# Kernel tuning notes

Hardware: AMD Instinct MI355X
Metric: run time of the kernel (lower is better)

The kernel has to match this reference:

```python
import jax, jax.numpy as jnp
import numpy as np

N_NODES = 50000
N_EDGES = 800000
IN_DIM = 128
HID = 64
HEADS = 4
OUT_DIM = 128
NEG_SLOPE = 0.2


def setup_inputs() -> dict:
    key = jax.random.key(0)
    ks = jax.random.split(key, 11)
    x = jax.random.normal(ks[0], (N_NODES, IN_DIM), dtype=jnp.float32)
    edge_index = jax.random.randint(ks[1], (2, N_EDGES), 0, N_NODES, dtype=jnp.int64)
    s1 = 1.0 / np.sqrt(IN_DIM)
    s2 = 1.0 / np.sqrt(HEADS * HID)
    W1 = jax.random.normal(ks[2], (IN_DIM, HEADS * HID), dtype=jnp.float32) * s1
    a_src1 = jax.random.normal(ks[3], (HEADS, HID), dtype=jnp.float32) * s2
    a_dst1 = jax.random.normal(ks[4], (HEADS, HID), dtype=jnp.float32) * s2
    b1 = jnp.zeros((HEADS * HID,), dtype=jnp.float32)
    W2 = jax.random.normal(ks[5], (HEADS * HID, OUT_DIM), dtype=jnp.float32) * s2
    a_src2 = jax.random.normal(ks[6], (1, OUT_DIM), dtype=jnp.float32) * 0.1
    a_dst2 = jax.random.normal(ks[7], (1, OUT_DIM), dtype=jnp.float32) * 0.1
    b2 = jnp.zeros((OUT_DIM,), dtype=jnp.float32)
    return {"x": x, "edge_index": edge_index, "W1": W1, "a_src1": a_src1,
            "a_dst1": a_dst1, "b1": b1, "W2": W2, "a_src2": a_src2,
            "a_dst2": a_dst2, "b2": b2}


def _gat_conv(x, src, dst, W, a_src, a_dst, bias, heads, out_per_head, concat):
    n = x.shape[0]
    # linear projection per head: [N, H, F]
    h = (x @ W).reshape(n, heads, out_per_head)
    # per-node attention terms: [N, H]
    alpha_src = jnp.einsum('nhf,hf->nh', h, a_src)
    alpha_dst = jnp.einsum('nhf,hf->nh', h, a_dst)
    # edge logits with LeakyReLU: [E, H]
    e = jax.nn.leaky_relu(alpha_src[src] + alpha_dst[dst], NEG_SLOPE)
    # softmax over incoming edges of each destination node
    m = jax.ops.segment_max(e, dst, num_segments=n)  # [N, H]
    m = jnp.where(jnp.isfinite(m), m, 0.0)
    e = jnp.exp(e - m[dst])
    denom = jax.ops.segment_sum(e, dst, num_segments=n)  # [N, H]
    alpha = e / (denom[dst] + 1e-16)  # [E, H]
    # weighted scatter-aggregate of source messages
    out = jax.ops.segment_sum(h[src] * alpha[:, :, None], dst, num_segments=n)  # [N, H, F]
    if concat:
        out = out.reshape(n, heads * out_per_head)
    else:
        out = out.mean(axis=1)
    return out + bias


def reference(x, edge_index, W1, a_src1, a_dst1, b1, W2, a_src2, a_dst2, b2):
    n = x.shape[0]
    # PyG GATConv adds self-loops by default
    loops = jnp.arange(n, dtype=edge_index.dtype)
    src = jnp.concatenate([edge_index[0], loops])
    dst = jnp.concatenate([edge_index[1], loops])
    # dropout layers are identity in inference
    h = _gat_conv(x, src, dst, W1, a_src1, a_dst1, b1, HEADS, HID, True)
    h = jax.nn.elu(h)
    out = _gat_conv(h, src, dst, W2, a_src2, a_dst2, b2, 1, OUT_DIM, True)
    # F.normalize(p=2, dim=1)
    norm = jnp.linalg.norm(out, axis=1, keepdims=True)
    return out / jnp.maximum(norm, 1e-12)
```

## Files before the change

### kernel.cpp

```cpp
#include <hip/hip_runtime.h>
#include <hip/hip_fp16.h>
#include <math.h>

#define N_NODES 50000
#define N_EDGES 800000
#define ET (N_EDGES + N_NODES)
#define IN_DIM 128
#define HID 64
#define HEADS 4
#define C1 (HEADS * HID)
#define OUT_DIM 128
#define NEG_SLOPE 0.2f
#define MTILES 3125
#define SCAN_B 1024
#define NSCB 49

typedef _Float16 h8 __attribute__((ext_vector_type(8)));
typedef float f4 __attribute__((ext_vector_type(4)));
typedef unsigned short u16;

__device__ __forceinline__ float leaky(float v) { return fmaxf(v, NEG_SLOPE * v); }
__device__ __forceinline__ float elu(float v) { return v > 0.0f ? v : expm1f(v); }

__device__ __forceinline__ void fma_mix8(float* acc, h8 v, float w) {
    union { h8 h; int i[4]; } u; u.h = v;
#pragma unroll
    for (int k = 0; k < 4; ++k) {
        asm("v_fma_mix_f32 %0, %1, %2, %0 op_sel:[0,0,0] op_sel_hi:[1,0,0]"
            : "+v"(acc[2 * k]) : "v"(u.i[k]), "v"(w));
        asm("v_fma_mix_f32 %0, %1, %2, %0 op_sel:[1,0,0] op_sel_hi:[1,0,0]"
            : "+v"(acc[2 * k + 1]) : "v"(u.i[k]), "v"(w));
    }
}

__global__ void prep_kernel(const float* __restrict__ W1, const float* __restrict__ W2,
                            const int* __restrict__ dst, __half* __restrict__ w1t,
                            __half* __restrict__ w2t, int* __restrict__ cnt,
                            u16* __restrict__ rank16) {
    const int tid = blockIdx.x * blockDim.x + threadIdx.x;
    const int np = gridDim.x * blockDim.x;
    for (int i = tid; i < IN_DIM * C1; i += np) {
        int k1 = i >> 8, n1 = i & 255;
        w1t[n1 * IN_DIM + k1] = __float2half(W1[i]);
        int k2 = i >> 7, n2 = i & 127;
        w2t[n2 * C1 + k2] = __float2half(W2[i]);
    }
    if (tid < N_EDGES / 4) {
        int4 d4 = ((const int4*)dst)[tid];
        int r0 = atomicAdd(&cnt[d4.x], 1);
        int r1 = atomicAdd(&cnt[d4.y], 1);
        int r2 = atomicAdd(&cnt[d4.z], 1);
        int r3 = atomicAdd(&cnt[d4.w], 1);
        ((ushort4*)rank16)[tid] = make_ushort4((u16)r0, (u16)r1, (u16)r2, (u16)r3);
    }
}

__global__ void scan_local(const int* __restrict__ cnt, int* __restrict__ lscan,
                           int* __restrict__ bsum) {
    __shared__ int wsum[16];
    const int t = threadIdx.x, lane = t & 63, wv = t >> 6;
    int idx = blockIdx.x * SCAN_B + t;
    int v = (idx < N_NODES) ? cnt[idx] + 1 : 0;
    int sc = v;
#pragma unroll
    for (int o = 1; o < 64; o <<= 1) {
        int u = __shfl_up(sc, o);
        if (lane >= o) sc += u;
    }
    if (lane == 63) wsum[wv] = sc;
    __syncthreads();
    if (t == 0) {
        int run = 0;
#pragma unroll
        for (int w = 0; w < 16; ++w) { int s = wsum[w]; wsum[w] = run; run += s; }
        bsum[blockIdx.x] = run;
    }
    __syncthreads();
    if (idx < N_NODES) lscan[idx] = sc + wsum[wv];
}

__global__ void scan_bsum(int* __restrict__ bsum) {
    const int t = threadIdx.x;
    int v = (t < NSCB) ? bsum[t] : 0;
    int sc = v;
#pragma unroll
    for (int o = 1; o < 64; o <<= 1) {
        int u = __shfl_up(sc, o);
        if (t >= o) sc += u;
    }
    if (t < NSCB) bsum[t] = sc - v;
}

__global__ void scan_final(const int* __restrict__ lscan, const int* __restrict__ bsum,
                           int* __restrict__ rp) {
    int idx = blockIdx.x * SCAN_B + threadIdx.x;
    if (idx == 0) rp[0] = 0;
    if (idx >= N_NODES) return;
    rp[idx + 1] = lscan[idx] + bsum[idx >> 10];
}

__global__ void scatter_plain(const int* __restrict__ src, const int* __restrict__ dst,
                              const u16* __restrict__ rank16, const int* __restrict__ rp,
                              u16* __restrict__ cs16) {
    const int tid = blockIdx.x * blockDim.x + threadIdx.x;
    if (tid < N_EDGES / 4) {
        int4 s4 = ((const int4*)src)[tid];
        int4 d4 = ((const int4*)dst)[tid];
        ushort4 r4 = ((const ushort4*)rank16)[tid];
        int p0 = rp[d4.x] + (int)r4.x;
        int p1 = rp[d4.y] + (int)r4.y;
        int p2 = rp[d4.z] + (int)r4.z;
        int p3 = rp[d4.w] + (int)r4.w;
        cs16[p0] = (u16)s4.x;
        cs16[p1] = (u16)s4.y;
        cs16[p2] = (u16)s4.z;
        cs16[p3] = (u16)s4.w;
    } else {
        int d = tid - N_EDGES / 4;
        if (d < N_NODES) cs16[rp[d + 1] - 1] = (u16)d;
    }
}

__global__ __launch_bounds__(256) void gemm1_mfma(
        const float* __restrict__ x, const __half* __restrict__ w1t,
        const float* __restrict__ aws, const float* __restrict__ awd,
        __half* __restrict__ hpm, float* __restrict__ as1m, float* __restrict__ ad1m) {
    const int tile = blockIdx.x * 4 + (threadIdx.x >> 6);
    if (tile >= MTILES) return;
    const int lane = threadIdx.x & 63;
    const int m0 = tile * 16, lm = lane & 15, lq = lane >> 4;
    h8 afrag[4];
    const float4* xrow = (const float4*)(x + (size_t)(m0 + lm) * IN_DIM + lq * 8);
#pragma unroll
    for (int kt = 0; kt < 4; ++kt) {
        float4 a = xrow[kt * 8];
        float4 b = xrow[kt * 8 + 1];
        union { h8 v; __half2 p[4]; } u;
        u.p[0] = __floats2half2_rn(a.x, a.y);
        u.p[1] = __floats2half2_rn(a.z, a.w);
        u.p[2] = __floats2half2_rn(b.x, b.y);
        u.p[3] = __floats2half2_rn(b.z, b.w);
        afrag[kt] = u.v;
    }
    f4 acc[16];
#pragma unroll
    for (int nt = 0; nt < 16; ++nt) acc[nt] = (f4){0.f, 0.f, 0.f, 0.f};
#pragma unroll
    for (int nt = 0; nt < 16; ++nt) {
        const h8* brow = (const h8*)(w1t + (size_t)(nt * 16 + lm) * IN_DIM + lq * 8);
#pragma unroll
        for (int kt = 0; kt < 4; ++kt)
            acc[nt] = __builtin_amdgcn_mfma_f32_16x16x32_f16(afrag[kt], brow[kt * 4],
                                                             acc[nt], 0, 0, 0);
    }
    float sS[4][4] = {{0.f}}, sD[4][4] = {{0.f}};
#pragma unroll
    for (int nt = 0; nt < 16; ++nt) {
        int col = nt * 16 + lm;
        float wa = aws[col], wd = awd[col];
        int hd = nt >> 2;
        int pr = nt >> 3;
        int cip = col & 127;
#pragma unroll
        for (int r = 0; r < 4; ++r) {
            float v = acc[nt][r];
            hpm[((size_t)pr * N_NODES + (m0 + lq * 4 + r)) * 128 + cip] = __float2half(v);
            sS[hd][r] += v * wa;
            sD[hd][r] += v * wd;
        }
    }
#pragma unroll
    for (int o = 1; o < 16; o <<= 1) {
#pragma unroll
        for (int hd = 0; hd < 4; ++hd)
#pragma unroll
            for (int r = 0; r < 4; ++r) {
                sS[hd][r] += __shfl_xor(sS[hd][r], o);
                sD[hd][r] += __shfl_xor(sD[hd][r], o);
            }
    }
    if (lm == 0) {
        float2* asp = (float2*)as1m;
        float2* adp = (float2*)ad1m;
#pragma unroll
        for (int r = 0; r < 4; ++r) {
            int row = m0 + lq * 4 + r;
            asp[row]           = make_float2(sS[0][r], sS[1][r]);
            asp[N_NODES + row] = make_float2(sS[2][r], sS[3][r]);
            adp[row]           = make_float2(sD[0][r], sD[1][r]);
            adp[N_NODES + row] = make_float2(sD[2][r], sD[3][r]);
        }
    }
}

__global__ __launch_bounds__(256) void gemm2_mfma(
        const __half* __restrict__ ah, const __half* __restrict__ w2t,
        const float* __restrict__ aws, const float* __restrict__ awd,
        __half* __restrict__ h, float* __restrict__ as2, float* __restrict__ ad2) {
    const int tile = blockIdx.x * 4 + (threadIdx.x >> 6);
    if (tile >= MTILES) return;
    const int lane = threadIdx.x & 63;
    const int m0 = tile * 16, lm = lane & 15, lq = lane >> 4;
    h8 afrag[8];
    const h8* arow = (const h8*)(ah + (size_t)(m0 + lm) * C1 + lq * 8);
#pragma unroll
    for (int kt = 0; kt < 8; ++kt) afrag[kt] = arow[kt * 4];
    f4 acc[8];
#pragma unroll
    for (int nt = 0; nt < 8; ++nt) acc[nt] = (f4){0.f, 0.f, 0.f, 0.f};
#pragma unroll
    for (int nt = 0; nt < 8; ++nt) {
        const h8* brow = (const h8*)(w2t + (size_t)(nt * 16 + lm) * C1 + lq * 8);
#pragma unroll
        for (int kt = 0; kt < 8; ++kt)
            acc[nt] = __builtin_amdgcn_mfma_f32_16x16x32_f16(afrag[kt], brow[kt * 4],
                                                             acc[nt], 0, 0, 0);
    }
    float sS[4] = {0.f, 0.f, 0.f, 0.f}, sD[4] = {0.f, 0.f, 0.f, 0.f};
#pragma unroll
    for (int nt = 0; nt < 8; ++nt) {
        int col = nt * 16 + lm;
        float wa = aws[col], wd = awd[col];
#pragma unroll
        for (int r = 0; r < 4; ++r) {
            float v = acc[nt][r];
            h[(size_t)(m0 + lq * 4 + r) * OUT_DIM + col] = __float2half(v);
            sS[r] += v * wa;
            sD[r] += v * wd;
        }
    }
#pragma unroll
    for (int o = 1; o < 16; o <<= 1) {
#pragma unroll
        for (int r = 0; r < 4; ++r) {
            sS[r] += __shfl_xor(sS[r], o);
            sD[r] += __shfl_xor(sD[r], o);
        }
    }
    if (lm == 0) {
#pragma unroll
        for (int r = 0; r < 4; ++r) {
            int row = m0 + lq * 4 + r;
            as2[row] = sS[r];
            ad2[row] = sD[r];
        }
    }
}

__global__ __launch_bounds__(256) void aggregate1_fused(
        const int* __restrict__ rp, const u16* __restrict__ cs16,
        const __half* __restrict__ hpm, const float* __restrict__ as1m,
        const float* __restrict__ ad1m, const float* __restrict__ b1,
        __half* __restrict__ out1h) {
    __shared__ int4 stg[8][32];
    const int pair = blockIdx.x & 1, g = blockIdx.x >> 1;
    const int hw = threadIdx.x >> 5, li = threadIdx.x & 31;
    const int d = g * 8 + hw;
    const int e0 = rp[d], deg = rp[d + 1] - e0;
    const float2* asb = (const float2*)as1m + (size_t)pair * N_NODES;
    const float2 adv = ((const float2*)ad1m)[(size_t)pair * N_NODES + d];
    const char* hb = (const char*)hpm + (size_t)pair * N_NODES * 256;
    const int es = li >> 4, fl = li & 15;
    const int hip = fl >> 3;
    const int lbyte = fl * 16;
    float acc[8] = {0.f, 0.f, 0.f, 0.f, 0.f, 0.f, 0.f, 0.f};
    float ds0 = 0.f, ds1 = 0.f;
    for (int c0 = 0; c0 < deg; c0 += 32) {
        const int clen = min(32, deg - c0);
        int idx = c0 + li;
        bool valid = idx < deg;
        int s = valid ? (int)cs16[e0 + idx] : 0;
        float2 av = asb[s];
        float x0 = valid ? __expf(leaky(av.x + adv.x)) : 0.f;
        float x1 = valid ? __expf(leaky(av.y + adv.y)) : 0.f;
        stg[hw][li] = make_int4(s << 8, __float_as_int(x0), __float_as_int(x1), 0);
        ds0 += x0; ds1 += x1;
        __builtin_amdgcn_wave_barrier();
        int j = 0;
        for (; j + 8 <= clen; j += 8) {
            int4 p0 = stg[hw][j + es];
            int4 p1 = stg[hw][j + 2 + es];
            int4 p2 = stg[hw][j + 4 + es];
            int4 p3 = stg[hw][j + 6 + es];
            h8 v0 = *(const h8*)(hb + p0.x + lbyte);
            h8 v1 = *(const h8*)(hb + p1.x + lbyte);
            h8 v2 = *(const h8*)(hb + p2.x + lbyte);
            h8 v3 = *(const h8*)(hb + p3.x + lbyte);
            fma_mix8(acc, v0, __int_as_float(hip ? p0.z : p0.y));
            fma_mix8(acc, v1, __int_as_float(hip ? p1.z : p1.y));
            fma_mix8(acc, v2, __int_as_float(hip ? p2.z : p2.y));
            fma_mix8(acc, v3, __int_as_float(hip ? p3.z : p3.y));
        }
        for (; j < clen; j += 2) {
            int4 p0 = stg[hw][j + es];
            h8 v0 = *(const h8*)(hb + p0.x + lbyte);
            fma_mix8(acc, v0, __int_as_float(hip ? p0.z : p0.y));
        }
        __builtin_amdgcn_wave_barrier();
    }
#pragma unroll
    for (int f = 0; f < 8; ++f) acc[f] += __shfl_xor(acc[f], 16);
#pragma unroll
    for (int o = 16; o > 0; o >>= 1) {
        ds0 += __shfl_xor(ds0, o);
        ds1 += __shfl_xor(ds1, o);
    }
    if (es == 0) {
        float den = hip ? ds1 : ds0;
        float inv = 1.0f / (den + 1e-16f);
        float4 bA = ((const float4*)b1)[pair * 32 + fl * 2];
        float4 bB = ((const float4*)b1)[pair * 32 + fl * 2 + 1];
        h8 o;
        o[0] = (_Float16)elu(acc[0] * inv + bA.x);
        o[1] = (_Float16)elu(acc[1] * inv + bA.y);
        o[2] = (_Float16)elu(acc[2] * inv + bA.z);
        o[3] = (_Float16)elu(acc[3] * inv + bA.w);
        o[4] = (_Float16)elu(acc[4] * inv + bB.x);
        o[5] = (_Float16)elu(acc[5] * inv + bB.y);
        o[6] = (_Float16)elu(acc[6] * inv + bB.z);
        o[7] = (_Float16)elu(acc[7] * inv + bB.w);
        *(h8*)((char*)out1h + (size_t)d * 512 + pair * 256 + lbyte) = o;
    }
}

__global__ __launch_bounds__(256) void aggregate2_fused(
        const int* __restrict__ rp, const u16* __restrict__ cs16,
        const __half* __restrict__ h2h, const float* __restrict__ as2,
        const float* __restrict__ ad2, const float* __restrict__ b2,
        float* __restrict__ out) {
    __shared__ int2 stg[8][32];
    const int hw = threadIdx.x >> 5, li = threadIdx.x & 31;
    const int d = blockIdx.x * 8 + hw;
    const int e0 = rp[d], deg = rp[d + 1] - e0;
    const float adv = ad2[d];
    const int q = li >> 4, lo = li & 15;
    const int lbyte = lo * 16;
    const char* hbase = (const char*)h2h;
    float acc[8] = {0.f, 0.f, 0.f, 0.f, 0.f, 0.f, 0.f, 0.f};
    float dsum = 0.f;
    for (int c0 = 0; c0 < deg; c0 += 32) {
        const int clen = min(32, deg - c0);
        int idx = c0 + li;
        bool valid = idx < deg;
        int s = valid ? (int)cs16[e0 + idx] : 0;
        float xv = valid ? __expf(leaky(as2[s] + adv)) : 0.f;
        stg[hw][li] = make_int2(s << 8, __float_as_int(xv));
        dsum += xv;
        __builtin_amdgcn_wave_barrier();
        int j = 0;
        for (; j + 8 <= clen; j += 8) {
            int2 p0 = stg[hw][j + q];
            int2 p1 = stg[hw][j + 2 + q];
            int2 p2 = stg[hw][j + 4 + q];
            int2 p3 = stg[hw][j + 6 + q];
            h8 v0 = *(const h8*)(hbase + p0.x + lbyte);
            h8 v1 = *(const h8*)(hbase + p1.x + lbyte);
            h8 v2 = *(const h8*)(hbase + p2.x + lbyte);
            h8 v3 = *(const h8*)(hbase + p3.x + lbyte);
            fma_mix8(acc, v0, __int_as_float(p0.y));
            fma_mix8(acc, v1, __int_as_float(p1.y));
            fma_mix8(acc, v2, __int_as_float(p2.y));
            fma_mix8(acc, v3, __int_as_float(p3.y));
        }
        for (; j < clen; j += 2) {
            int2 p0 = stg[hw][j + q];
            h8 v0 = *(const h8*)(hbase + p0.x + lbyte);
            fma_mix8(acc, v0, __int_as_float(p0.y));
        }
        __builtin_amdgcn_wave_barrier();
    }
#pragma unroll
    for (int f = 0; f < 8; ++f) acc[f] += __shfl_xor(acc[f], 16);
#pragma unroll
    for (int o = 16; o > 0; o >>= 1) dsum += __shfl_xor(dsum, o);
    if (q == 0) {
        float inv = 1.0f / (dsum + 1e-16f);
        float4 bA = ((const float4*)b2)[lo * 2];
        float4 bB = ((const float4*)b2)[lo * 2 + 1];
        float v0 = acc[0] * inv + bA.x, v1 = acc[1] * inv + bA.y;
        float v2 = acc[2] * inv + bA.z, v3 = acc[3] * inv + bA.w;
        float v4 = acc[4] * inv + bB.x, v5 = acc[5] * inv + bB.y;
        float v6 = acc[6] * inv + bB.z, v7 = acc[7] * inv + bB.w;
        float ss = v0 * v0 + v1 * v1 + v2 * v2 + v3 * v3 +
                   v4 * v4 + v5 * v5 + v6 * v6 + v7 * v7;
#pragma unroll
        for (int o = 1; o < 16; o <<= 1) ss += __shfl_xor(ss, o);
        float sc = 1.0f / fmaxf(sqrtf(ss), 1e-12f);
        float4* orow = (float4*)((char*)out + (size_t)d * 512 + lo * 32);
        orow[0] = make_float4(v0 * sc, v1 * sc, v2 * sc, v3 * sc);
        orow[1] = make_float4(v4 * sc, v5 * sc, v6 * sc, v7 * sc);
    }
}

extern "C" void kernel_launch(void* const* d_in, const int* in_sizes, int n_in,
                              void* d_out, int out_size, void* d_ws, size_t ws_size,
                              hipStream_t stream) {
    const float* x     = (const float*)d_in[0];
    const int*   edge  = (const int*)d_in[1];
    const int*   src   = edge;
    const int*   dst   = edge + N_EDGES;
    const float* W1    = (const float*)d_in[2];
    const float* aw_s1 = (const float*)d_in[3];
    const float* aw_d1 = (const float*)d_in[4];
    const float* b1    = (const float*)d_in[5];
    const float* W2    = (const float*)d_in[6];
    const float* aw_s2 = (const float*)d_in[7];
    const float* aw_d2 = (const float*)d_in[8];
    const float* b2    = (const float*)d_in[9];
    float* out = (float*)d_out;

    char* ws = (char*)d_ws;
    size_t off = 0;
    auto alloc = [&](size_t bytes) {
        void* p = ws + off;
        off += (bytes + 255) & ~(size_t)255;
        return p;
    };
    u16*    cs16   = (u16*)alloc((size_t)ET * 2);
    u16*    rank16 = (u16*)alloc((size_t)N_EDGES * 2);
    int*    rp     = (int*)alloc((size_t)(N_NODES + 1) * 4);
    int*    cnt    = (int*)alloc((size_t)N_NODES * 4);
    int*    lscan  = (int*)alloc((size_t)NSCB * SCAN_B * 4);
    int*    bsum   = (int*)alloc((size_t)NSCB * 4);
    float*  as1    = (float*)alloc((size_t)N_NODES * HEADS * 4);
    float*  ad1    = (float*)alloc((size_t)N_NODES * HEADS * 4);
    float*  as2    = (float*)alloc((size_t)N_NODES * 4);
    float*  ad2    = (float*)alloc((size_t)N_NODES * 4);
    __half* w1t    = (__half*)alloc((size_t)IN_DIM * C1 * 2);
    __half* w2t    = (__half*)alloc((size_t)C1 * OUT_DIM * 2);
    __half* hpm    = (__half*)alloc((size_t)N_NODES * C1 * 2);
    __half* out1h  = (__half*)alloc((size_t)N_NODES * C1 * 2);
    __half* h2h    = hpm;
    (void)off;

    hipMemsetAsync(cnt, 0, (size_t)N_NODES * 4, stream);

    prep_kernel<<<1024, 256, 0, stream>>>(W1, W2, dst, w1t, w2t, cnt, rank16);
    scan_local<<<NSCB, SCAN_B, 0, stream>>>(cnt, lscan, bsum);
    scan_bsum<<<1, 64, 0, stream>>>(bsum);
    scan_final<<<NSCB, SCAN_B, 0, stream>>>(lscan, bsum, rp);
    scatter_plain<<<(N_EDGES / 4 + N_NODES + 255) / 256, 256, 0, stream>>>(
        src, dst, rank16, rp, cs16);

    gemm1_mfma<<<(MTILES + 3) / 4, 256, 0, stream>>>(x, w1t, aw_s1, aw_d1, hpm, as1, ad1);
    aggregate1_fused<<<(N_NODES / 8) * 2, 256, 0, stream>>>(rp, cs16, hpm, as1, ad1, b1, out1h);

    gemm2_mfma<<<(MTILES + 3) / 4, 256, 0, stream>>>(out1h, w2t, aw_s2, aw_d2, h2h, as2, ad2);
    aggregate2_fused<<<N_NODES / 8, 256, 0, stream>>>(rp, cs16, h2h, as2, ad2, b2, out);
}
```

Baseline: 310.7 us.

## Replace global atomic degree count with per-block LDS histograms

Edge destinations are now counted with 64 blocks, each building a packed 16-bit LDS histogram over its slice of edges in two halves of the node range. Local ranks come from the shared-memory atomics. scan_local then prefix-sums across the 64 per-block count rows to get per-block offsets, and the scatter adds those offsets. This drops the global atomics and the memset, at the cost of only 64 blocks doing the histogram work (low parallelism) and roughly 12.8 MB of extra count and offset traffic.

Measured after the change: 312.2 us. Within noise of the previous version (+0.5%).

```diff
diff --git a/kernel.cpp b/kernel.cpp
--- a/kernel.cpp
+++ b/kernel.cpp
@@ -14,6 +14,8 @@
 #define MTILES 3125
 #define SCAN_B 1024
 #define NSCB 49
+#define HB 64
+#define EPB (N_EDGES / HB)
 
 typedef _Float16 h8 __attribute__((ext_vector_type(8)));
 typedef float f4 __attribute__((ext_vector_type(4)));
@@ -33,34 +35,54 @@
     }
 }
 
-__global__ void prep_kernel(const float* __restrict__ W1, const float* __restrict__ W2,
-                            const int* __restrict__ dst, __half* __restrict__ w1t,
-                            __half* __restrict__ w2t, int* __restrict__ cnt,
-                            u16* __restrict__ rank16) {
-    const int tid = blockIdx.x * blockDim.x + threadIdx.x;
-    const int np = gridDim.x * blockDim.x;
-    for (int i = tid; i < IN_DIM * C1; i += np) {
+__global__ __launch_bounds__(256) void hist_kernel(
+        const float* __restrict__ W1, const float* __restrict__ W2,
+        const int* __restrict__ dst, __half* __restrict__ w1t,
+        __half* __restrict__ w2t, u16* __restrict__ cnt_mat,
+        u16* __restrict__ lrank16) {
+    __shared__ unsigned pk[N_NODES / 4];
+    const int b = blockIdx.x, t = threadIdx.x;
+    for (int i = b * 256 + t; i < IN_DIM * C1; i += HB * 256) {
         int k1 = i >> 8, n1 = i & 255;
         w1t[n1 * IN_DIM + k1] = __float2half(W1[i]);
         int k2 = i >> 7, n2 = i & 127;
         w2t[n2 * C1 + k2] = __float2half(W2[i]);
     }
-    if (tid < N_EDGES / 4) {
-        int4 d4 = ((const int4*)dst)[tid];
-        int r0 = atomicAdd(&cnt[d4.x], 1);
-        int r1 = atomicAdd(&cnt[d4.y], 1);
-        int r2 = atomicAdd(&cnt[d4.z], 1);
-        int r3 = atomicAdd(&cnt[d4.w], 1);
-        ((ushort4*)rank16)[tid] = make_ushort4((u16)r0, (u16)r1, (u16)r2, (u16)r3);
-    }
-}
-
-__global__ void scan_local(const int* __restrict__ cnt, int* __restrict__ lscan,
-                           int* __restrict__ bsum) {
+    const int e0 = b * EPB;
+#pragma unroll
+    for (int half = 0; half < 2; ++half) {
+        const int nbase = half * (N_NODES / 2);
+        for (int i = t; i < N_NODES / 4; i += 256) pk[i] = 0;
+        __syncthreads();
+        for (int k = t; k < EPB; k += 256) {
+            int d = dst[e0 + k] - nbase;
+            if ((unsigned)d < (unsigned)(N_NODES / 2)) {
+                unsigned r = atomicAdd(&pk[d >> 1], (d & 1) ? 65536u : 1u);
+                lrank16[e0 + k] = (u16)((d & 1) ? (r >> 16) : (r & 0xffffu));
+            }
+        }
+        __syncthreads();
+        unsigned* crow = (unsigned*)(cnt_mat + (size_t)b * N_NODES) + half * (N_NODES / 4);
+        for (int i = t; i < N_NODES / 4; i += 256) crow[i] = pk[i];
+        __syncthreads();
+    }
+}
+
+__global__ void scan_local(const u16* __restrict__ cnt_mat, u16* __restrict__ boff,
+                           int* __restrict__ lscan, int* __restrict__ bsum) {
     __shared__ int wsum[16];
     const int t = threadIdx.x, lane = t & 63, wv = t >> 6;
     int idx = blockIdx.x * SCAN_B + t;
-    int v = (idx < N_NODES) ? cnt[idx] + 1 : 0;
+    int run = 0;
+    if (idx < N_NODES) {
+#pragma unroll 8
+        for (int b = 0; b < HB; ++b) {
+            u16 c = cnt_mat[(size_t)b * N_NODES + idx];
+            boff[(size_t)b * N_NODES + idx] = (u16)run;
+            run += c;
+        }
+    }
+    int v = (idx < N_NODES) ? run + 1 : 0;
     int sc = v;
 #pragma unroll
     for (int o = 1; o < 64; o <<= 1) {
@@ -70,10 +92,10 @@
     if (lane == 63) wsum[wv] = sc;
     __syncthreads();
     if (t == 0) {
-        int run = 0;
-#pragma unroll
-        for (int w = 0; w < 16; ++w) { int s = wsum[w]; wsum[w] = run; run += s; }
-        bsum[blockIdx.x] = run;
+        int run2 = 0;
+#pragma unroll
+        for (int w = 0; w < 16; ++w) { int s = wsum[w]; wsum[w] = run2; run2 += s; }
+        bsum[blockIdx.x] = run2;
     }
     __syncthreads();
     if (idx < N_NODES) lscan[idx] = sc + wsum[wv];
@@ -100,21 +122,19 @@
 }
 
 __global__ void scatter_plain(const int* __restrict__ src, const int* __restrict__ dst,
-                              const u16* __restrict__ rank16, const int* __restrict__ rp,
-                              u16* __restrict__ cs16) {
+                              const u16* __restrict__ lrank16, const u16* __restrict__ boff,
+                              const int* __restrict__ rp, u16* __restrict__ cs16) {
     const int tid = blockIdx.x * blockDim.x + threadIdx.x;
     if (tid < N_EDGES / 4) {
+        const int b = tid / (EPB / 4);
+        const u16* bo = boff + (size_t)b * N_NODES;
         int4 s4 = ((const int4*)src)[tid];
         int4 d4 = ((const int4*)dst)[tid];
-        ushort4 r4 = ((const ushort4*)rank16)[tid];
-        int p0 = rp[d4.x] + (int)r4.x;
-        int p1 = rp[d4.y] + (int)r4.y;
-        int p2 = rp[d4.z] + (int)r4.z;
-        int p3 = rp[d4.w] + (int)r4.w;
-        cs16[p0] = (u16)s4.x;
-        cs16[p1] = (u16)s4.y;
-        cs16[p2] = (u16)s4.z;
-        cs16[p3] = (u16)s4.w;
+        ushort4 r4 = ((const ushort4*)lrank16)[tid];
+        cs16[rp[d4.x] + (int)bo[d4.x] + (int)r4.x] = (u16)s4.x;
+        cs16[rp[d4.y] + (int)bo[d4.y] + (int)r4.y] = (u16)s4.y;
+        cs16[rp[d4.z] + (int)bo[d4.z] + (int)r4.z] = (u16)s4.z;
+        cs16[rp[d4.w] + (int)bo[d4.w] + (int)r4.w] = (u16)s4.w;
     } else {
         int d = tid - N_EDGES / 4;
         if (d < N_NODES) cs16[rp[d + 1] - 1] = (u16)d;
@@ -416,31 +436,31 @@
         off += (bytes + 255) & ~(size_t)255;
         return p;
     };
-    u16*    cs16   = (u16*)alloc((size_t)ET * 2);
-    u16*    rank16 = (u16*)alloc((size_t)N_EDGES * 2);
-    int*    rp     = (int*)alloc((size_t)(N_NODES + 1) * 4);
-    int*    cnt    = (int*)alloc((size_t)N_NODES * 4);
-    int*    lscan  = (int*)alloc((size_t)NSCB * SCAN_B * 4);
-    int*    bsum   = (int*)alloc((size_t)NSCB * 4);
-    float*  as1    = (float*)alloc((size_t)N_NODES * HEADS * 4);
-    float*  ad1    = (float*)alloc((size_t)N_NODES * HEADS * 4);
-    float*  as2    = (float*)alloc((size_t)N_NODES * 4);
-    float*  ad2    = (float*)alloc((size_t)N_NODES * 4);
-    __half* w1t    = (__half*)alloc((size_t)IN_DIM * C1 * 2);
-    __half* w2t    = (__half*)alloc((size_t)C1 * OUT_DIM * 2);
-    __half* hpm    = (__half*)alloc((size_t)N_NODES * C1 * 2);
-    __half* out1h  = (__half*)alloc((size_t)N_NODES * C1 * 2);
-    __half* h2h    = hpm;
+    u16*    cs16    = (u16*)alloc((size_t)ET * 2);
+    u16*    lrank16 = (u16*)alloc((size_t)N_EDGES * 2);
+    u16*    cnt_mat = (u16*)alloc((size_t)HB * N_NODES * 2);
+    u16*    boff    = (u16*)alloc((size_t)HB * N_NODES * 2);
+    int*    rp      = (int*)alloc((size_t)(N_NODES + 1) * 4);
+    int*    lscan   = (int*)alloc((size_t)NSCB * SCAN_B * 4);
+    int*    bsum    = (int*)alloc((size_t)NSCB * 4);
+    float*  as1     = (float*)alloc((size_t)N_NODES * HEADS * 4);
+    float*  ad1     = (float*)alloc((size_t)N_NODES * HEADS * 4);
+    float*  as2     = (float*)alloc((size_t)N_NODES * 4);
+    float*  ad2     = (float*)alloc((size_t)N_NODES * 4);
+    __half* w1t     = (__half*)alloc((size_t)IN_DIM * C1 * 2);
+    __half* w2t     = (__half*)alloc((size_t)C1 * OUT_DIM * 2);
+    __half* hpm     = (__half*)alloc((size_t)N_NODES * C1 * 2);
+    __half* out1h   = (__half*)alloc((size_t)N_NODES * C1 * 2);
+    __half* h2h     = hpm;
     (void)off;
 
-    hipMemsetAsync(cnt, 0, (size_t)N_NODES * 4, stream);
-
-    prep_kernel<<<1024, 256, 0, stream>>>(W1, W2, dst, w1t, w2t, cnt, rank16);
-    scan_local<<<NSCB, SCAN_B, 0, stream>>>(cnt, lscan, bsum);
+
+    hist_kernel<<<HB, 256, 0, stream>>>(W1, W2, dst, w1t, w2t, cnt_mat, lrank16);
+    scan_local<<<NSCB, SCAN_B, 0, stream>>>(cnt_mat, boff, lscan, bsum);
     scan_bsum<<<1, 64, 0, stream>>>(bsum);
     scan_final<<<NSCB, SCAN_B, 0, stream>>>(lscan, bsum, rp);
     scatter_plain<<<(N_EDGES / 4 + N_NODES + 255) / 256, 256, 0, stream>>>(
-        src, dst, rank16, rp, cs16);
+        src, dst, lrank16, boff, rp, cs16);
 
     gemm1_mfma<<<(MTILES + 3) / 4, 256, 0, stream>>>(x, w1t, aw_s1, aw_d1, hpm, as1, ad1);
     aggregate1_fused<<<(N_NODES / 8) * 2, 256, 0, stream>>>(rp, cs16, hpm, as1, ad1, b1, out1h);
```
